# Kernel tuning notes

Hardware: AMD Instinct MI355X
Metric: run time of the kernel (lower is better)

Reference implementation:

```python
import jax, jax.numpy as jnp
import numpy as np

N_NODES = 20000
OUT_DEG = 16
E = N_NODES * OUT_DEG          # 320000 directed edges
F = 20                          # edge_features
H3 = 3 * F


def _lin(key, fan_in, fan_out):
    kw, kb = jax.random.split(key)
    bound = 1.0 / np.sqrt(fan_in)
    W = jax.random.uniform(kw, (fan_in, fan_out), jnp.float32, -bound, bound)
    b = jax.random.uniform(kb, (fan_out,), jnp.float32, -bound, bound)
    return W, b


def setup_inputs() -> dict:
    key = jax.random.key(0)
    rng = np.random.default_rng(0)
    # graph: every node has exactly OUT_DEG out-edges, no self-loops
    src = np.repeat(np.arange(N_NODES, dtype=np.int64), OUT_DEG)
    dst = (src + 1 + rng.integers(0, N_NODES - 1, size=E)) % N_NODES
    edge_index = jnp.asarray(np.stack([src, dst]), dtype=jnp.int32)
    # edge adjacency per _build_edge_adj: edge i=(u->v) pairs with each out-edge j of v.
    # Edges are grouped by src, so out-edges of node v are [v*OUT_DEG, v*OUT_DEG+OUT_DEG).
    # No self-loops => i != j always, so exactly E*OUT_DEG pairs.
    adj_src = jnp.asarray(np.repeat(np.arange(E, dtype=np.int64), OUT_DEG).astype(np.int32))
    adj_nbr = jnp.asarray((dst[:, None] * OUT_DEG + np.arange(OUT_DEG)).reshape(-1).astype(np.int32))

    ks = jax.random.split(key, 8)
    edge_attr = jax.random.normal(ks[0], (E, F), jnp.float32)
    msg_W1, msg_b1 = _lin(ks[1], 2 * F, 32)
    msg_W2, msg_b2 = _lin(ks[2], 32, F)
    # torch GRUCell params: weight_ih/hh are [3H, H]
    bound = 1.0 / np.sqrt(F)
    g = jax.random.split(ks[3], 4)
    gru_Wih = jax.random.uniform(g[0], (H3, F), jnp.float32, -bound, bound)
    gru_Whh = jax.random.uniform(g[1], (H3, F), jnp.float32, -bound, bound)
    gru_bih = jax.random.uniform(g[2], (H3,), jnp.float32, -bound, bound)
    gru_bhh = jax.random.uniform(g[3], (H3,), jnp.float32, -bound, bound)
    ro_W1, ro_b1 = _lin(ks[4], F, 64)
    ro_W2, ro_b2 = _lin(ks[5], 64, 32)
    ro_W3, ro_b3 = _lin(ks[6], 32, 1)
    return {
        'edge_attr': edge_attr,
        'msg_W1': msg_W1, 'msg_b1': msg_b1, 'msg_W2': msg_W2, 'msg_b2': msg_b2,
        'gru_Wih': gru_Wih, 'gru_Whh': gru_Whh, 'gru_bih': gru_bih, 'gru_bhh': gru_bhh,
        'ro_W1': ro_W1, 'ro_b1': ro_b1, 'ro_W2': ro_W2, 'ro_b2': ro_b2,
        'ro_W3': ro_W3, 'ro_b3': ro_b3,
        'edge_index': edge_index, 'adj_src': adj_src, 'adj_nbr': adj_nbr,
    }


def reference(edge_attr, msg_W1, msg_b1, msg_W2, msg_b2,
              gru_Wih, gru_Whh, gru_bih, gru_bhh,
              ro_W1, ro_b1, ro_W2, ro_b2, ro_W3, ro_b3,
              edge_index, adj_src, adj_nbr):
    num_e = edge_attr.shape[0]

    def step(h, _):
        h_i = h[adj_src]                       # [P, F] gather
        h_j = h[adj_nbr]                       # [P, F] gather
        m = jnp.concatenate([h_i, h_j], axis=-1)  # [P, 2F]
        m = jax.nn.selu(m @ msg_W1 + msg_b1) @ msg_W2 + msg_b2  # [P, F]
        agg = jax.ops.segment_sum(m, adj_src, num_segments=num_e)  # scatter_add
        # torch.nn.GRUCell(agg, h)
        gi = agg @ gru_Wih.T + gru_bih
        gh = h @ gru_Whh.T + gru_bhh
        i_r, i_z, i_n = jnp.split(gi, 3, axis=-1)
        h_r, h_z, h_n = jnp.split(gh, 3, axis=-1)
        r = jax.nn.sigmoid(i_r + h_r)
        z = jax.nn.sigmoid(i_z + h_z)
        n = jnp.tanh(i_n + r * h_n)
        return (1.0 - z) * n + z * h, None

    h_t, _ = jax.lax.scan(step, edge_attr, None, length=4)
    h_base = h_t[:num_e]  # num_edges == E here
    x = jax.nn.selu(h_base @ ro_W1 + ro_b1)
    x = jax.nn.selu(x @ ro_W2 + ro_b2)
    w = jax.nn.softplus(x @ ro_W3 + ro_b3).squeeze(-1) + 0.1
    return jnp.clip(w, 0.1, 10.0)
```

## Files before the change

kernel.cpp:

```cpp
#include <hip/hip_runtime.h>
#include <hip/hip_fp16.h>

#define E_EDGES 320000
#define NF 20

typedef float v4 __attribute__((ext_vector_type(4)));
typedef float v2f __attribute__((ext_vector_type(2)));

#if defined(__has_builtin)
# if __has_builtin(__builtin_elementwise_fma)
#  define EWFMA(a,b,c) __builtin_elementwise_fma((a),(b),(c))
# endif
#endif
#ifndef EWFMA
# define EWFMA(a,b,c) ((a)*(b)+(c))
#endif
#if defined(__has_builtin)
# if __has_builtin(__builtin_elementwise_max)
#  define EWMAX(a,b) __builtin_elementwise_max((a),(b))
#  define EWMIN(a,b) __builtin_elementwise_min((a),(b))
# endif
#endif

__device__ __forceinline__ v4 bc4(float s) { return (v4){s, s, s, s}; }
__device__ __forceinline__ v4 v4z() { return (v4){0.f, 0.f, 0.f, 0.f}; }

__device__ __forceinline__ float selu_f(float x) {
    const float scale = 1.0507009873554805f;
    const float alpha = 1.6732632423543772f;
    float p = fmaxf(x, 0.f);
    float m = fminf(x, 0.f);
    float e = __expf(m);
    return fmaf(scale, p, scale * alpha * (e - 1.f));
}
__device__ __forceinline__ float sigmoid_f(float x) {
    return 1.f / (1.f + __expf(-x));
}
__device__ __forceinline__ v4 selu4(v4 x) {
    const float scale = 1.0507009873554805f;
    const float ka = 1.0507009873554805f * 1.6732632423543772f;
#ifdef EWMAX
    v4 p = EWMAX(x, v4z());
    v4 m = EWMIN(x, v4z());
#else
    v4 p = {fmaxf(x.x,0.f), fmaxf(x.y,0.f), fmaxf(x.z,0.f), fmaxf(x.w,0.f)};
    v4 m = {fminf(x.x,0.f), fminf(x.y,0.f), fminf(x.z,0.f), fminf(x.w,0.f)};
#endif
    v4 e = {__expf(m.x), __expf(m.y), __expf(m.z), __expf(m.w)};
    return EWFMA(bc4(scale), p, EWFMA(bc4(ka), e, bc4(-ka)));
}

__device__ __forceinline__ float hsum4(v4 x) {
    v2f lo = __builtin_shufflevector(x, x, 0, 1);
    v2f hi = __builtin_shufflevector(x, x, 2, 3);
    v2f h = lo + hi;
    return h.x + h.y;
}

__device__ __forceinline__ float dot20v(v4 a0, v4 a1, v4 a2, v4 a3, v4 a4,
                                        const v4* __restrict__ w) {
    v4 w0 = w[0], w1 = w[1], w2 = w[2], w3 = w[3], w4 = w[4];
    v4 x = a0 * w0;
    x = EWFMA(a1, w1, x); x = EWFMA(a2, w2, x);
    x = EWFMA(a3, w3, x); x = EWFMA(a4, w4, x);
    return hsum4(x);
}
__device__ __forceinline__ void dot20_dualv(const v4* __restrict__ w,
    v4 a0, v4 a1, v4 a2, v4 a3, v4 a4,
    v4 b0, v4 b1, v4 b2, v4 b3, v4 b4,
    float& r0, float& r1)
{
    v4 w0 = w[0], w1 = w[1], w2 = w[2], w3 = w[3], w4 = w[4];
    v4 xa = a0 * w0;
    xa = EWFMA(a1, w1, xa); xa = EWFMA(a2, w2, xa);
    xa = EWFMA(a3, w3, xa); xa = EWFMA(a4, w4, xa);
    v4 xb = b0 * w0;
    xb = EWFMA(b1, w1, xb); xb = EWFMA(b2, w2, xb);
    xb = EWFMA(b3, w3, xb); xb = EWFMA(b4, w4, xb);
    r0 = hsum4(xa);
    r1 = hsum4(xb);
}
__device__ __forceinline__ void h8_to_v4x2(uint4 r, v4& lo, v4& hi) {
    float2 fa = __half22float2(__builtin_bit_cast(__half2, r.x));
    float2 fb = __half22float2(__builtin_bit_cast(__half2, r.y));
    float2 fc = __half22float2(__builtin_bit_cast(__half2, r.z));
    float2 fd = __half22float2(__builtin_bit_cast(__half2, r.w));
    lo = (v4){fa.x, fa.y, fb.x, fb.y};
    hi = (v4){fc.x, fc.y, fd.x, fd.y};
}
__device__ __forceinline__ uint4 f8_to_h8(v4 lo, v4 hi) {
    uint4 r;
    r.x = __builtin_bit_cast(unsigned, __floats2half2_rn(lo.x, lo.y));
    r.y = __builtin_bit_cast(unsigned, __floats2half2_rn(lo.z, lo.w));
    r.z = __builtin_bit_cast(unsigned, __floats2half2_rn(hi.x, hi.y));
    r.w = __builtin_bit_cast(unsigned, __floats2half2_rn(hi.z, hi.w));
    return r;
}

#define FOR20(X) \
  X(0, v0.x) X(1, v0.y) X(2, v0.z) X(3, v0.w) \
  X(4, v1.x) X(5, v1.y) X(6, v1.z) X(7, v1.w) \
  X(8, v2.x) X(9, v2.y) X(10, v2.z) X(11, v2.w) \
  X(12, v3.x) X(13, v3.y) X(14, v3.z) X(15, v3.w) \
  X(16, v4v.x) X(17, v4v.y) X(18, v4v.z) X(19, v4v.w)

#define FOR20_2(X) \
  X(0, va0.x, vb0.x) X(1, va0.y, vb0.y) X(2, va0.z, vb0.z) X(3, va0.w, vb0.w) \
  X(4, va1.x, vb1.x) X(5, va1.y, vb1.y) X(6, va1.z, vb1.z) X(7, va1.w, vb1.w) \
  X(8, va2.x, vb2.x) X(9, va2.y, vb2.y) X(10, va2.z, vb2.z) X(11, va2.w, vb2.w) \
  X(12, va3.x, vb3.x) X(13, va3.y, vb3.y) X(14, va3.z, vb3.z) X(15, va3.w, vb3.w) \
  X(16, va4.x, vb4.x) X(17, va4.y, vb4.y) X(18, va4.z, vb4.z) X(19, va4.w, vb4.w)

#define FOR8S2(X) \
  X(0, sa0.x, sb0.x) X(1, sa0.y, sb0.y) X(2, sa0.z, sb0.z) X(3, sa0.w, sb0.w) \
  X(4, sa1.x, sb1.x) X(5, sa1.y, sb1.y) X(6, sa1.z, sb1.z) X(7, sa1.w, sb1.w)

__global__ void __launch_bounds__(256) kernel_B0(
    const float* __restrict__ h, const float* __restrict__ W1,
    const float* __restrict__ b1, __half* __restrict__ B)
{
    __shared__ __align__(16) float sw[640];
    __shared__ __align__(16) float sbias[32];
    for (int i = threadIdx.x; i < 640; i += 256) sw[i] = W1[640 + i];
    if (threadIdx.x < 32) sbias[threadIdx.x] = b1[threadIdx.x];
    __syncthreads();
    int e = blockIdx.x * 256 + threadIdx.x;
    const v4* hp = reinterpret_cast<const v4*>(h + (size_t)e * NF);
    v4 v0 = hp[0], v1 = hp[1], v2 = hp[2], v3 = hp[3], v4v = hp[4];
    const v4* bi = reinterpret_cast<const v4*>(sbias);
    v4 c0 = bi[0], c1 = bi[1], c2 = bi[2], c3 = bi[3],
       c4 = bi[4], c5 = bi[5], c6 = bi[6], c7 = bi[7];
    #define BSTEP(f, hf) { v4 t_ = bc4(hf); const v4* w_ = (const v4*)&sw[(f)*32]; \
        c0 = EWFMA(t_, w_[0], c0); c1 = EWFMA(t_, w_[1], c1); \
        c2 = EWFMA(t_, w_[2], c2); c3 = EWFMA(t_, w_[3], c3); \
        c4 = EWFMA(t_, w_[4], c4); c5 = EWFMA(t_, w_[5], c5); \
        c6 = EWFMA(t_, w_[6], c6); c7 = EWFMA(t_, w_[7], c7); }
    FOR20(BSTEP)
    #undef BSTEP
    uint4* Bp = reinterpret_cast<uint4*>(B + (size_t)e * 32);
    Bp[0] = f8_to_h8(c0, c1); Bp[1] = f8_to_h8(c2, c3);
    Bp[2] = f8_to_h8(c4, c5); Bp[3] = f8_to_h8(c6, c7);
}

__global__ void __launch_bounds__(256) kernel_step(
    const float* __restrict__ h_in, float* __restrict__ h_out,
    const __half* __restrict__ Br, const int* __restrict__ dst,
    const float* __restrict__ W1, const float* __restrict__ W2, const float* __restrict__ b2,
    const float* __restrict__ Wih, const float* __restrict__ Whh,
    const float* __restrict__ bih, const float* __restrict__ bhh)
{
    __shared__ __align__(16) float sW1[640];
    __shared__ __align__(16) float sW2[640];
    __shared__ __align__(16) float sb2v[20];
    __shared__ __align__(16) float sWih[1200];
    __shared__ __align__(16) float sWhh[1200];
    __shared__ float sbih[60];
    __shared__ float sbhh[60];
    for (int i = threadIdx.x; i < 640; i += 256) { sW1[i] = W1[i]; sW2[i] = W2[i]; }
    for (int i = threadIdx.x; i < 1200; i += 256) { sWih[i] = Wih[i]; sWhh[i] = Whh[i]; }
    if (threadIdx.x < 20) sb2v[threadIdx.x] = b2[threadIdx.x];
    else if (threadIdx.x >= 64 && threadIdx.x < 124) sbih[threadIdx.x - 64] = bih[threadIdx.x - 64];
    else if (threadIdx.x >= 128 && threadIdx.x < 188) sbhh[threadIdx.x - 128] = bhh[threadIdx.x - 128];
    __syncthreads();

    int t = blockIdx.x * 256 + threadIdx.x;
    int p = t >> 2;
    int q = t & 3;
    int ob = q * 8;
    int e0 = p * 2, e1 = p * 2 + 1;

    int2 dd = *reinterpret_cast<const int2*>(dst + e0);
    int d0 = dd.x, d1 = dd.y;

    const v4* hp0 = reinterpret_cast<const v4*>(h_in + (size_t)e0 * NF);
    const v4* hp1 = reinterpret_cast<const v4*>(h_in + (size_t)e1 * NF);
    v4 va0 = hp0[0], va1 = hp0[1], va2 = hp0[2], va3 = hp0[3], va4 = hp0[4];
    v4 vb0 = hp1[0], vb1 = hp1[1], vb2 = hp1[2], vb3 = hp1[3], vb4 = hp1[4];

    v4 aa0 = v4z(), aa1 = v4z(), ab0 = v4z(), ab1 = v4z();
    #define ASTEP2(f, h0, h1) { const v4* w_ = (const v4*)&sW1[(f)*32 + ob]; \
        v4 w0_ = w_[0], w1_ = w_[1]; \
        v4 t0_ = bc4(h0), t1_ = bc4(h1); \
        aa0 = EWFMA(t0_, w0_, aa0); aa1 = EWFMA(t0_, w1_, aa1); \
        ab0 = EWFMA(t1_, w0_, ab0); ab1 = EWFMA(t1_, w1_, ab1); }
    FOR20_2(ASTEP2)
    #undef ASTEP2

    const uint4* Bp0 = reinterpret_cast<const uint4*>(Br) + (size_t)d0 * 64 + q;
    const uint4* Bp1 = reinterpret_cast<const uint4*>(Br) + (size_t)d1 * 64 + q;
    v4 sa0 = v4z(), sa1 = v4z(), sb0 = v4z(), sb1 = v4z();
    #pragma unroll 4
    for (int k = 0; k < 16; k++) {
        uint4 rA = Bp0[k * 4];
        uint4 rB = Bp1[k * 4];
        v4 loA, hiA, loB, hiB;
        h8_to_v4x2(rA, loA, hiA);
        h8_to_v4x2(rB, loB, hiB);
        sa0 = sa0 + selu4(aa0 + loA);
        sa1 = sa1 + selu4(aa1 + hiA);
        sb0 = sb0 + selu4(ab0 + loB);
        sb1 = sb1 + selu4(ab1 + hiB);
    }

    v4 ga0 = v4z(), ga1 = v4z(), ga2 = v4z(), ga3 = v4z(), ga4 = v4z();
    v4 gb0 = v4z(), gb1 = v4z(), gb2 = v4z(), gb3 = v4z(), gb4 = v4z();
    #define AGGS2(j, c0_, c1_) { const v4* w_ = (const v4*)&sW2[(ob + (j)) * 20]; \
        v4 w0_ = w_[0], w1_ = w_[1], w2_ = w_[2], w3_ = w_[3], w4_ = w_[4]; \
        v4 u_ = bc4(c0_), vv_ = bc4(c1_); \
        ga0 = EWFMA(u_, w0_, ga0); ga1 = EWFMA(u_, w1_, ga1); ga2 = EWFMA(u_, w2_, ga2); \
        ga3 = EWFMA(u_, w3_, ga3); ga4 = EWFMA(u_, w4_, ga4); \
        gb0 = EWFMA(vv_, w0_, gb0); gb1 = EWFMA(vv_, w1_, gb1); gb2 = EWFMA(vv_, w2_, gb2); \
        gb3 = EWFMA(vv_, w3_, gb3); gb4 = EWFMA(vv_, w4_, gb4); }
    FOR8S2(AGGS2)
    #undef AGGS2

    #define BF1(r_, m_) { v4 t_ = { __shfl_xor(r_.x, m_), __shfl_xor(r_.y, m_), \
                                    __shfl_xor(r_.z, m_), __shfl_xor(r_.w, m_) }; \
                          r_ = r_ + t_; }
    #define BFLY(m_) BF1(ga0, m_) BF1(ga1, m_) BF1(ga2, m_) BF1(ga3, m_) BF1(ga4, m_) \
                     BF1(gb0, m_) BF1(gb1, m_) BF1(gb2, m_) BF1(gb3, m_) BF1(gb4, m_)
    BFLY(1)
    BFLY(2)
    #undef BFLY
    #undef BF1

    {
        const v4* b2p = reinterpret_cast<const v4*>(sb2v);
        v4 sixteen = bc4(16.f);
        v4 c0 = b2p[0], c1 = b2p[1], c2 = b2p[2], c3 = b2p[3], c4 = b2p[4];
        ga0 = EWFMA(sixteen, c0, ga0); ga1 = EWFMA(sixteen, c1, ga1); ga2 = EWFMA(sixteen, c2, ga2);
        ga3 = EWFMA(sixteen, c3, ga3); ga4 = EWFMA(sixteen, c4, ga4);
        gb0 = EWFMA(sixteen, c0, gb0); gb1 = EWFMA(sixteen, c1, gb1); gb2 = EWFMA(sixteen, c2, gb2);
        gb3 = EWFMA(sixteen, c3, gb3); gb4 = EWFMA(sixteen, c4, gb4);
    }

    for (int i = 0; i < 5; i++) {
        int c = q * 5 + i;
        float ir0, ir1, iz0, iz1, in0, in1, hr0, hr1, hz0, hz1, hn0, hn1;
        dot20_dualv((const v4*)&sWih[c * 20],        ga0, ga1, ga2, ga3, ga4,
                    gb0, gb1, gb2, gb3, gb4, ir0, ir1);
        dot20_dualv((const v4*)&sWih[(20 + c) * 20], ga0, ga1, ga2, ga3, ga4,
                    gb0, gb1, gb2, gb3, gb4, iz0, iz1);
        dot20_dualv((const v4*)&sWih[(40 + c) * 20], ga0, ga1, ga2, ga3, ga4,
                    gb0, gb1, gb2, gb3, gb4, in0, in1);
        dot20_dualv((const v4*)&sWhh[c * 20],        va0, va1, va2, va3, va4,
                    vb0, vb1, vb2, vb3, vb4, hr0, hr1);
        dot20_dualv((const v4*)&sWhh[(20 + c) * 20], va0, va1, va2, va3, va4,
                    vb0, vb1, vb2, vb3, vb4, hz0, hz1);
        dot20_dualv((const v4*)&sWhh[(40 + c) * 20], va0, va1, va2, va3, va4,
                    vb0, vb1, vb2, vb3, vb4, hn0, hn1);
        float bi_r = sbih[c], bi_z = sbih[20 + c], bi_n = sbih[40 + c];
        float bh_r = sbhh[c], bh_z = sbhh[20 + c], bh_n = sbhh[40 + c];
        {
            float r = sigmoid_f(bi_r + ir0 + bh_r + hr0);
            float z = sigmoid_f(bi_z + iz0 + bh_z + hz0);
            float xn = bi_n + in0 + r * (bh_n + hn0);
            xn = fminf(fmaxf(xn, -20.f), 20.f);
            float tt = __expf(2.f * xn);
            float n = (tt - 1.f) / (tt + 1.f);
            float hc = h_in[(size_t)e0 * NF + c];
            h_out[(size_t)e0 * NF + c] = (1.f - z) * n + z * hc;
        }
        {
            float r = sigmoid_f(bi_r + ir1 + bh_r + hr1);
            float z = sigmoid_f(bi_z + iz1 + bh_z + hz1);
            float xn = bi_n + in1 + r * (bh_n + hn1);
            xn = fminf(fmaxf(xn, -20.f), 20.f);
            float tt = __expf(2.f * xn);
            float n = (tt - 1.f) / (tt + 1.f);
            float hc = h_in[(size_t)e1 * NF + c];
            h_out[(size_t)e1 * NF + c] = (1.f - z) * n + z * hc;
        }
    }
}

__global__ void __launch_bounds__(256) kernel_readout(
    const float* __restrict__ h,
    const float* __restrict__ W1, const float* __restrict__ b1,
    const float* __restrict__ W2, const float* __restrict__ b2,
    const float* __restrict__ W3, const float* __restrict__ b3,
    float* __restrict__ out)
{
    __shared__ __align__(16) float sW1t[1280];
    __shared__ float sb1[64];
    __shared__ __align__(16) float sW2[2048];
    __shared__ __align__(16) float sb2v[32];
    __shared__ __align__(16) float sW3[32];
    __shared__ float sb3;
    for (int i = threadIdx.x; i < 1280; i += 256) {
        int f = i >> 6, o = i & 63;
        sW1t[o * 20 + f] = W1[i];
    }
    for (int i = threadIdx.x; i < 2048; i += 256) sW2[i] = W2[i];
    if (threadIdx.x < 64) sb1[threadIdx.x] = b1[threadIdx.x];
    else if (threadIdx.x >= 64 && threadIdx.x < 96) sb2v[threadIdx.x - 64] = b2[threadIdx.x - 64];
    else if (threadIdx.x >= 96 && threadIdx.x < 128) sW3[threadIdx.x - 96] = W3[threadIdx.x - 96];
    if (threadIdx.x == 128) sb3 = b3[0];
    __syncthreads();

    int e = blockIdx.x * 256 + threadIdx.x;
    const v4* hp = reinterpret_cast<const v4*>(h + (size_t)e * NF);
    v4 v0 = hp[0], v1 = hp[1], v2 = hp[2], v3 = hp[3], v4v = hp[4];

    const v4* b2p = reinterpret_cast<const v4*>(sb2v);
    v4 x20 = b2p[0], x21 = b2p[1], x22 = b2p[2], x23 = b2p[3],
       x24 = b2p[4], x25 = b2p[5], x26 = b2p[6], x27 = b2p[7];
    for (int o = 0; o < 64; o++) {
        float x1 = sb1[o] + dot20v(v0, v1, v2, v3, v4v, (const v4*)&sW1t[o * 20]);
        x1 = selu_f(x1);
        v4 xb = bc4(x1);
        const v4* w = (const v4*)&sW2[o * 32];
        x20 = EWFMA(xb, w[0], x20); x21 = EWFMA(xb, w[1], x21);
        x22 = EWFMA(xb, w[2], x22); x23 = EWFMA(xb, w[3], x23);
        x24 = EWFMA(xb, w[4], x24); x25 = EWFMA(xb, w[5], x25);
        x26 = EWFMA(xb, w[6], x26); x27 = EWFMA(xb, w[7], x27);
    }
    const v4* w3p = reinterpret_cast<const v4*>(sW3);
    v4 accv = selu4(x20) * w3p[0];
    accv = EWFMA(selu4(x21), w3p[1], accv);
    accv = EWFMA(selu4(x22), w3p[2], accv);
    accv = EWFMA(selu4(x23), w3p[3], accv);
    accv = EWFMA(selu4(x24), w3p[4], accv);
    accv = EWFMA(selu4(x25), w3p[5], accv);
    accv = EWFMA(selu4(x26), w3p[6], accv);
    accv = EWFMA(selu4(x27), w3p[7], accv);
    float acc = sb3 + hsum4(accv);
    float sp = fmaxf(acc, 0.f) + log1pf(__expf(-fabsf(acc)));
    float w = sp + 0.1f;
    w = fminf(fmaxf(w, 0.1f), 10.f);
    out[e] = w;
}

extern "C" void kernel_launch(void* const* d_in, const int* in_sizes, int n_in,
                              void* d_out, int out_size, void* d_ws, size_t ws_size,
                              hipStream_t stream) {
    const float* edge_attr = (const float*)d_in[0];
    const float* msg_W1   = (const float*)d_in[1];
    const float* msg_b1   = (const float*)d_in[2];
    const float* msg_W2   = (const float*)d_in[3];
    const float* msg_b2   = (const float*)d_in[4];
    const float* gru_Wih  = (const float*)d_in[5];
    const float* gru_Whh  = (const float*)d_in[6];
    const float* gru_bih  = (const float*)d_in[7];
    const float* gru_bhh  = (const float*)d_in[8];
    const float* ro_W1    = (const float*)d_in[9];
    const float* ro_b1    = (const float*)d_in[10];
    const float* ro_W2    = (const float*)d_in[11];
    const float* ro_b2    = (const float*)d_in[12];
    const float* ro_W3    = (const float*)d_in[13];
    const float* ro_b3    = (const float*)d_in[14];
    const int* edge_index = (const int*)d_in[15];
    const int* dst = edge_index + E_EDGES;

    float*  h_ws = (float*)d_ws;
    __half* Bt   = (__half*)(h_ws + (size_t)E_EDGES * NF);

    dim3 block(256);
    dim3 gridB(E_EDGES / 256);
    dim3 gridS(E_EDGES * 2 / 256);

    const float* hin = edge_attr;
    for (int s = 0; s < 4; s++) {
        kernel_B0<<<gridB, block, 0, stream>>>(hin, msg_W1, msg_b1, Bt);
        kernel_step<<<gridS, block, 0, stream>>>(hin, h_ws, Bt, dst,
            msg_W1, msg_W2, msg_b2, gru_Wih, gru_Whh, gru_bih, gru_bhh);
        hin = h_ws;
    }
    kernel_readout<<<gridB, block, 0, stream>>>(h_ws, ro_W1, ro_b1, ro_W2, ro_b2,
                                                ro_W3, ro_b3, (float*)d_out);
}
```

Before: 606.7 us.

## Fuse next-step message precompute into GRU step and simplify SELU with exp2

The step kernel now computes the half-precision W1 projection of the new hidden state in its epilogue, gathering hidden values across lanes with shuffles. It writes that projection into a double-buffered workspace, so the separate B0 kernel runs only once, before the first step. This removes three launches plus a full re-read of h and the B writes. Separately, W1 and b1 are pre-scaled by log2(e) so SELU can use a raw exp2, and the constant SELU offset is folded into a per-feature correction term. That cuts work in the 16-neighbour inner loop. The fused path depends on the workspace being large enough for two B buffers, and it adds register and shared-memory pressure to the step kernel.

Result: faster. 554.8 us (-8.6%).

```diff
diff --git a/kernel.cpp b/kernel.cpp
--- a/kernel.cpp
+++ b/kernel.cpp
@@ -22,12 +22,27 @@
 # endif
 #endif
 
+#if defined(__has_builtin)
+# if __has_builtin(__builtin_amdgcn_exp2f)
+#  define EX2F(x) __builtin_amdgcn_exp2f(x)
+# endif
+#endif
+#ifndef EX2F
+# define EX2F(x) exp2f(x)
+#endif
+
+#define LOG2E_F 1.4426950408889634f
+#define SELU_SCALE 1.0507009873554805f
+#define SELU_ALPHA 1.6732632423543772f
+#define SELU_KA (SELU_SCALE * SELU_ALPHA)
+#define SELU_SC2 (SELU_SCALE / LOG2E_F)
+
 __device__ __forceinline__ v4 bc4(float s) { return (v4){s, s, s, s}; }
 __device__ __forceinline__ v4 v4z() { return (v4){0.f, 0.f, 0.f, 0.f}; }
 
 __device__ __forceinline__ float selu_f(float x) {
-    const float scale = 1.0507009873554805f;
-    const float alpha = 1.6732632423543772f;
+    const float scale = SELU_SCALE;
+    const float alpha = SELU_ALPHA;
     float p = fmaxf(x, 0.f);
     float m = fminf(x, 0.f);
     float e = __expf(m);
@@ -37,8 +52,8 @@
     return 1.f / (1.f + __expf(-x));
 }
 __device__ __forceinline__ v4 selu4(v4 x) {
-    const float scale = 1.0507009873554805f;
-    const float ka = 1.0507009873554805f * 1.6732632423543772f;
+    const float scale = SELU_SCALE;
+    const float ka = SELU_KA;
 #ifdef EWMAX
     v4 p = EWMAX(x, v4z());
     v4 m = EWMIN(x, v4z());
@@ -121,8 +136,8 @@
 {
     __shared__ __align__(16) float sw[640];
     __shared__ __align__(16) float sbias[32];
-    for (int i = threadIdx.x; i < 640; i += 256) sw[i] = W1[640 + i];
-    if (threadIdx.x < 32) sbias[threadIdx.x] = b1[threadIdx.x];
+    for (int i = threadIdx.x; i < 640; i += 256) sw[i] = W1[640 + i] * LOG2E_F;
+    if (threadIdx.x < 32) sbias[threadIdx.x] = b1[threadIdx.x] * LOG2E_F;
     __syncthreads();
     int e = blockIdx.x * 256 + threadIdx.x;
     const v4* hp = reinterpret_cast<const v4*>(h + (size_t)e * NF);
@@ -142,25 +157,44 @@
     Bp[2] = f8_to_h8(c4, c5); Bp[3] = f8_to_h8(c6, c7);
 }
 
-__global__ void __launch_bounds__(256) kernel_step(
+template<bool WRITEB>
+__global__ void __launch_bounds__(256) kernel_stepT(
     const float* __restrict__ h_in, float* __restrict__ h_out,
     const __half* __restrict__ Br, const int* __restrict__ dst,
-    const float* __restrict__ W1, const float* __restrict__ W2, const float* __restrict__ b2,
+    const float* __restrict__ W1, const float* __restrict__ b1,
+    const float* __restrict__ W2, const float* __restrict__ b2,
     const float* __restrict__ Wih, const float* __restrict__ Whh,
-    const float* __restrict__ bih, const float* __restrict__ bhh)
+    const float* __restrict__ bih, const float* __restrict__ bhh,
+    __half* __restrict__ Bw)
 {
     __shared__ __align__(16) float sW1[640];
+    __shared__ __align__(16) float sW1h[640];
+    __shared__ __align__(16) float sb1h[32];
     __shared__ __align__(16) float sW2[640];
     __shared__ __align__(16) float sb2v[20];
+    __shared__ __align__(16) float sCorr[20];
     __shared__ __align__(16) float sWih[1200];
     __shared__ __align__(16) float sWhh[1200];
     __shared__ float sbih[60];
     __shared__ float sbhh[60];
-    for (int i = threadIdx.x; i < 640; i += 256) { sW1[i] = W1[i]; sW2[i] = W2[i]; }
+    for (int i = threadIdx.x; i < 640; i += 256) {
+        sW1[i] = W1[i] * LOG2E_F;
+        sW2[i] = W2[i];
+        if (WRITEB) sW1h[i] = W1[640 + i] * LOG2E_F;
+    }
     for (int i = threadIdx.x; i < 1200; i += 256) { sWih[i] = Wih[i]; sWhh[i] = Whh[i]; }
     if (threadIdx.x < 20) sb2v[threadIdx.x] = b2[threadIdx.x];
     else if (threadIdx.x >= 64 && threadIdx.x < 124) sbih[threadIdx.x - 64] = bih[threadIdx.x - 64];
     else if (threadIdx.x >= 128 && threadIdx.x < 188) sbhh[threadIdx.x - 128] = bhh[threadIdx.x - 128];
+    else if (WRITEB && threadIdx.x >= 192 && threadIdx.x < 224)
+        sb1h[threadIdx.x - 192] = b1[threadIdx.x - 192] * LOG2E_F;
+    __syncthreads();
+    if (threadIdx.x < 20) {
+        float s = 0.f;
+        #pragma unroll
+        for (int o = 0; o < 32; o++) s += sW2[o * 20 + threadIdx.x];
+        sCorr[threadIdx.x] = 16.f * (sb2v[threadIdx.x] - SELU_KA * s);
+    }
     __syncthreads();
 
     int t = blockIdx.x * 256 + threadIdx.x;
@@ -189,17 +223,25 @@
     const uint4* Bp0 = reinterpret_cast<const uint4*>(Br) + (size_t)d0 * 64 + q;
     const uint4* Bp1 = reinterpret_cast<const uint4*>(Br) + (size_t)d1 * 64 + q;
     v4 sa0 = v4z(), sa1 = v4z(), sb0 = v4z(), sb1 = v4z();
-    #pragma unroll 4
-    for (int k = 0; k < 16; k++) {
-        uint4 rA = Bp0[k * 4];
-        uint4 rB = Bp1[k * 4];
-        v4 loA, hiA, loB, hiB;
-        h8_to_v4x2(rA, loA, hiA);
-        h8_to_v4x2(rB, loB, hiB);
-        sa0 = sa0 + selu4(aa0 + loA);
-        sa1 = sa1 + selu4(aa1 + hiA);
-        sb0 = sb0 + selu4(ab0 + loB);
-        sb1 = sb1 + selu4(ab1 + hiB);
+    {
+        v4 kav = bc4(SELU_KA), scv = bc4(SELU_SC2), z4 = v4z();
+        #define SELUACC(s_, a_, b_) { v4 x_ = (a_) + (b_); \
+            v4 p_ = EWMAX(x_, z4); v4 m_ = EWMIN(x_, z4); \
+            v4 e_ = {EX2F(m_.x), EX2F(m_.y), EX2F(m_.z), EX2F(m_.w)}; \
+            s_ = EWFMA(kav, e_, s_); s_ = EWFMA(scv, p_, s_); }
+        #pragma unroll 4
+        for (int k = 0; k < 16; k++) {
+            uint4 rA = Bp0[k * 4];
+            uint4 rB = Bp1[k * 4];
+            v4 loA, hiA, loB, hiB;
+            h8_to_v4x2(rA, loA, hiA);
+            h8_to_v4x2(rB, loB, hiB);
+            SELUACC(sa0, aa0, loA);
+            SELUACC(sa1, aa1, hiA);
+            SELUACC(sb0, ab0, loB);
+            SELUACC(sb1, ab1, hiB);
+        }
+        #undef SELUACC
     }
 
     v4 ga0 = v4z(), ga1 = v4z(), ga2 = v4z(), ga3 = v4z(), ga4 = v4z();
@@ -225,13 +267,17 @@
     #undef BF1
 
     {
-        const v4* b2p = reinterpret_cast<const v4*>(sb2v);
-        v4 sixteen = bc4(16.f);
-        v4 c0 = b2p[0], c1 = b2p[1], c2 = b2p[2], c3 = b2p[3], c4 = b2p[4];
-        ga0 = EWFMA(sixteen, c0, ga0); ga1 = EWFMA(sixteen, c1, ga1); ga2 = EWFMA(sixteen, c2, ga2);
-        ga3 = EWFMA(sixteen, c3, ga3); ga4 = EWFMA(sixteen, c4, ga4);
-        gb0 = EWFMA(sixteen, c0, gb0); gb1 = EWFMA(sixteen, c1, gb1); gb2 = EWFMA(sixteen, c2, gb2);
-        gb3 = EWFMA(sixteen, c3, gb3); gb4 = EWFMA(sixteen, c4, gb4);
+        const v4* cp = reinterpret_cast<const v4*>(sCorr);
+        v4 c0 = cp[0], c1 = cp[1], c2 = cp[2], c3 = cp[3], c4 = cp[4];
+        ga0 = ga0 + c0; ga1 = ga1 + c1; ga2 = ga2 + c2; ga3 = ga3 + c3; ga4 = ga4 + c4;
+        gb0 = gb0 + c0; gb1 = gb1 + c1; gb2 = gb2 + c2; gb3 = gb3 + c3; gb4 = gb4 + c4;
+    }
+
+    v4 ba0, ba1, bb0, bb1;
+    if (WRITEB) {
+        const v4* b1p = reinterpret_cast<const v4*>(&sb1h[ob]);
+        ba0 = b1p[0]; ba1 = b1p[1];
+        bb0 = b1p[0]; bb1 = b1p[1];
     }
 
     for (int i = 0; i < 5; i++) {
@@ -251,6 +297,7 @@
                     vb0, vb1, vb2, vb3, vb4, hn0, hn1);
         float bi_r = sbih[c], bi_z = sbih[20 + c], bi_n = sbih[40 + c];
         float bh_r = sbhh[c], bh_z = sbhh[20 + c], bh_n = sbhh[40 + c];
+        float nh0, nh1;
         {
             float r = sigmoid_f(bi_r + ir0 + bh_r + hr0);
             float z = sigmoid_f(bi_z + iz0 + bh_z + hz0);
@@ -259,7 +306,8 @@
             float tt = __expf(2.f * xn);
             float n = (tt - 1.f) / (tt + 1.f);
             float hc = h_in[(size_t)e0 * NF + c];
-            h_out[(size_t)e0 * NF + c] = (1.f - z) * n + z * hc;
+            nh0 = (1.f - z) * n + z * hc;
+            h_out[(size_t)e0 * NF + c] = nh0;
         }
         {
             float r = sigmoid_f(bi_r + ir1 + bh_r + hr1);
@@ -269,8 +317,26 @@
             float tt = __expf(2.f * xn);
             float n = (tt - 1.f) / (tt + 1.f);
             float hc = h_in[(size_t)e1 * NF + c];
-            h_out[(size_t)e1 * NF + c] = (1.f - z) * n + z * hc;
+            nh1 = (1.f - z) * n + z * hc;
+            h_out[(size_t)e1 * NF + c] = nh1;
         }
+        if (WRITEB) {
+            #pragma unroll
+            for (int qq = 0; qq < 4; ++qq) {
+                float f0 = __shfl(nh0, qq, 4);
+                float f1 = __shfl(nh1, qq, 4);
+                const v4* wp = reinterpret_cast<const v4*>(&sW1h[(qq * 5 + i) * 32 + ob]);
+                v4 w0 = wp[0], w1 = wp[1];
+                v4 t0 = bc4(f0), t1 = bc4(f1);
+                ba0 = EWFMA(t0, w0, ba0); ba1 = EWFMA(t0, w1, ba1);
+                bb0 = EWFMA(t1, w0, bb0); bb1 = EWFMA(t1, w1, bb1);
+            }
+        }
+    }
+    if (WRITEB) {
+        uint4* Bo = reinterpret_cast<uint4*>(Bw);
+        Bo[(size_t)e0 * 4 + q] = f8_to_h8(ba0, ba1);
+        Bo[(size_t)e1 * 4 + q] = f8_to_h8(bb0, bb1);
     }
 }
 
@@ -353,17 +419,35 @@
     const int* dst = edge_index + E_EDGES;
 
     float*  h_ws = (float*)d_ws;
-    __half* Bt   = (__half*)(h_ws + (size_t)E_EDGES * NF);
+    __half* BtA  = (__half*)(h_ws + (size_t)E_EDGES * NF);
+    __half* BtB  = BtA + (size_t)E_EDGES * 32;
+
+    size_t need = (size_t)E_EDGES * NF * sizeof(float)
+                + 2 * (size_t)E_EDGES * 32 * sizeof(__half);
+    bool fused = ws_size >= need;
 
     dim3 block(256);
     dim3 gridB(E_EDGES / 256);
     dim3 gridS(E_EDGES * 2 / 256);
 
+    kernel_B0<<<gridB, block, 0, stream>>>(edge_attr, msg_W1, msg_b1, BtA);
+
     const float* hin = edge_attr;
+    __half* Bin = BtA;
+    __half* Bout = BtB;
     for (int s = 0; s < 4; s++) {
-        kernel_B0<<<gridB, block, 0, stream>>>(hin, msg_W1, msg_b1, Bt);
-        kernel_step<<<gridS, block, 0, stream>>>(hin, h_ws, Bt, dst,
-            msg_W1, msg_W2, msg_b2, gru_Wih, gru_Whh, gru_bih, gru_bhh);
+        if (!fused && s > 0)
+            kernel_B0<<<gridB, block, 0, stream>>>(hin, msg_W1, msg_b1, BtA);
+        if (fused && s < 3) {
+            kernel_stepT<true><<<gridS, block, 0, stream>>>(hin, h_ws, Bin, dst,
+                msg_W1, msg_b1, msg_W2, msg_b2, gru_Wih, gru_Whh, gru_bih, gru_bhh,
+                Bout);
+            __half* tmp = Bin; Bin = Bout; Bout = tmp;
+        } else {
+            kernel_stepT<false><<<gridS, block, 0, stream>>>(hin, h_ws, Bin, dst,
+                msg_W1, msg_b1, msg_W2, msg_b2, gru_Wih, gru_Whh, gru_bih, gru_bhh,
+                nullptr);
+        }
         hin = h_ws;
     }
     kernel_readout<<<gridB, block, 0, stream>>>(h_ws, ro_W1, ro_b1, ro_W2, ro_b2,
```
